# Kernel optimization log

Hardware: AMD Instinct MI355X
Metric: run time of the kernel (lower is better)

## Reference

```python
import jax, jax.numpy as jnp
import numpy as np
from jax import lax

K = 13  # sizearea
DN = ('NCHW', 'OIHW', 'NCHW')


def conv(x, W, b):
    y = lax.conv_general_dilated(x, W, (1, 1), 'SAME', dimension_numbers=DN)
    return y + b[None, :, None, None]


def setup_inputs() -> dict:
    key = jax.random.key(0)
    ks = jax.random.split(key, 4)
    x = jax.random.normal(ks[0], (8, 1, 256, 256), dtype=jnp.float32)
    W1 = jax.random.normal(ks[1], (64, 1, 3, 3), dtype=jnp.float32) * 0.1
    b1 = jnp.zeros((64,), dtype=jnp.float32)
    W2 = jax.random.normal(ks[2], (64, 64, 3, 3), dtype=jnp.float32) * 0.05
    b2 = jnp.zeros((64,), dtype=jnp.float32)
    W3 = jax.random.normal(ks[3], (K * K, 64, 3, 3), dtype=jnp.float32) * 0.05
    b3 = jnp.zeros((K * K,), dtype=jnp.float32)
    return {'x': x, 'W1': W1, 'b1': b1, 'W2': W2, 'b2': b2, 'W3': W3, 'b3': b3}


def reference(x, W1, b1, W2, b2, W3, b3):
    # weight-predicting CNN (sar_data=False -> x used directly)
    h = jax.nn.relu(conv(x, W1, b1))
    h = jax.nn.relu(conv(h, W2, b2))
    w = conv(h, W3, b3)                       # (B, K*K, H, W)

    B, C, H, Wd = x.shape                     # C == 1
    # w.permute(0,2,3,1).view(B,1,H,W,K,K)
    wr = jnp.transpose(w, (0, 2, 3, 1)).reshape(B, 1, H, Wd, K, K)

    Ho, Wo = H - K + 1, Wd - K + 1            # unfold with stride 1, no pad
    pr, pc = (H - Ho) // 2, (Wd - Wo) // 2    # center-crop of weight maps
    wc = wr[:, :, pr:H - pr, pc:Wd - pc]      # (B,1,Ho,Wo,K,K)

    # patches[b,0,i,j,u,v] = x[b,0,i+u,j+v]  (C=1, so channel-major flatten is just (kh,kw))
    patches = lax.conv_general_dilated_patches(
        x, (K, K), (1, 1), 'VALID', dimension_numbers=DN)   # (B, K*K, Ho, Wo)
    patches = patches.reshape(B, 1, K, K, Ho, Wo).transpose(0, 1, 4, 5, 2, 3)

    # per-pixel weighted sum over the KxK window
    y = jnp.einsum('bchwuv,bchwuv->bchw', patches, wc)       # (B,1,Ho,Wo)
    return y
```

## Files before the change

### kernel.cpp

```cpp
#include <hip/hip_runtime.h>

#define HW 256
#define BATCH 8
#define C 64
#define HO 244
#define NPAD 192
#define KTOT 576

typedef __bf16 bf16x8 __attribute__((ext_vector_type(8)));
typedef float f32x16 __attribute__((ext_vector_type(16)));
typedef float f32x2 __attribute__((ext_vector_type(2)));
typedef unsigned short us8 __attribute__((ext_vector_type(8)));

__device__ inline unsigned short fbf(float f) {
    return __builtin_bit_cast(unsigned short, (__bf16)f);
}

__device__ inline float bf2f(unsigned short s) {
    union { unsigned int u; float f; } c;
    c.u = ((unsigned int)s) << 16;
    return c.f;
}

__global__ __launch_bounds__(256) void repack_w_kernel(
    const float* __restrict__ W2, const float* __restrict__ W3,
    unsigned short* __restrict__ B2g, unsigned short* __restrict__ B3g)
{
    int idx = blockIdx.x * 256 + threadIdx.x;
    if (idx < 36 * 2 * C * 8) {
        int e = idx & 7;
        int r = idx >> 3;
        int n = r & 63;
        int s = r >> 6;
        int khalf = s & 1;
        int kstep = s >> 1;
        int chunk = kstep >> 2, ks = kstep & 3;
        int ci = ks * 16 + khalf * 8 + e;
        B2g[idx] = fbf(W2[((size_t)n * C + ci) * 9 + chunk]);
    } else {
        int j = idx - 36 * 2 * C * 8;
        if (j >= 36 * 2 * NPAD * 8) return;
        int e = j & 7;
        int r = j >> 3;
        int n = r % NPAD;
        int s = r / NPAD;
        int khalf = s & 1;
        int kstep = s >> 1;
        int chunk = kstep >> 2, ks = kstep & 3;
        int ci = ks * 16 + khalf * 8 + e;
        float v = (n < 169) ? W3[((size_t)n * C + ci) * 9 + chunk] : 0.f;
        B3g[j] = fbf(v);
    }
}

__global__ __launch_bounds__(256, 3) void conv2_fused_kernel(
    const float* __restrict__ x, const float* __restrict__ W1,
    const float* __restrict__ b1, const unsigned short* __restrict__ W2r,
    const float* __restrict__ b2, unsigned short* __restrict__ h2)
{
    __shared__ unsigned short Ash[396 * 66];
    __shared__ unsigned short Xsh[8 * 68];

    const int t = threadIdx.x;
    const int lane = t & 63;
    const int wave = t >> 6;
    const int b  = blockIdx.z;
    const int h0 = blockIdx.y * 4;
    const int w0 = blockIdx.x * 64;

    const int col   = lane & 31;
    const int khalf = lane >> 5;
    const int mrow_base = wave * 64;

    const float* __restrict__ xplane = x + ((size_t)b << 16);
#pragma unroll
    for (int it = 0; it < 3; ++it) {
        int li = it * 256 + t;
        if (li < 8 * 68) {
            int rr = li / 68, cc = li - rr * 68;
            int hh = h0 - 2 + rr, ww = w0 - 2 + cc;
            bool ok = (hh >= 0) && (hh < HW) && (ww >= 0) && (ww < HW);
            Xsh[li] = ok ? fbf(xplane[hh * HW + ww]) : (unsigned short)0;
        }
    }

    const int g4 = t & 15;
    f32x2 w01[9], w23[9];
    f32x2 bia01, bia23;
    bia01[0] = b1[g4 * 4 + 0]; bia01[1] = b1[g4 * 4 + 1];
    bia23[0] = b1[g4 * 4 + 2]; bia23[1] = b1[g4 * 4 + 3];
#pragma unroll
    for (int q = 0; q < 9; ++q) {
        w01[q][0] = W1[(g4 * 4 + 0) * 9 + q];
        w01[q][1] = W1[(g4 * 4 + 1) * 9 + q];
        w23[q][0] = W1[(g4 * 4 + 2) * 9 + q];
        w23[q][1] = W1[(g4 * 4 + 3) * 9 + q];
    }

    __syncthreads();

    for (int it = 0; it < 25; ++it) {
        int li = it * 256 + t;
        if (li < 6336) {
            int p = li >> 4;
            int pr = p / 66, pc = p - pr * 66;
            int hh = h0 - 1 + pr, ww = w0 - 1 + pc;
            unsigned short ov[4];
            if (hh >= 0 && hh < HW && ww >= 0 && ww < HW) {
                const unsigned short* xb = Xsh + pr * 68 + pc;
                f32x2 a01 = bia01, a23 = bia23;
#pragma unroll
                for (int i = 0; i < 3; ++i)
#pragma unroll
                    for (int j = 0; j < 3; ++j) {
                        float xv = bf2f(xb[i * 68 + j]);
                        f32x2 xv2; xv2[0] = xv; xv2[1] = xv;
                        a01 += xv2 * w01[i * 3 + j];
                        a23 += xv2 * w23[i * 3 + j];
                    }
                ov[0] = fbf(fmaxf(a01[0], 0.f));
                ov[1] = fbf(fmaxf(a01[1], 0.f));
                ov[2] = fbf(fmaxf(a23[0], 0.f));
                ov[3] = fbf(fmaxf(a23[1], 0.f));
            } else {
#pragma unroll
                for (int u = 0; u < 4; ++u) ov[u] = 0;
            }
            *(uint2*)(Ash + p * 66 + g4 * 4) = *(uint2*)ov;
        }
    }

    const unsigned short* bbase = W2r + ((size_t)khalf * C + col) * 8;
    us8 bcur0 = *(const us8*)(bbase);
    us8 bcur1 = *(const us8*)(bbase + 32 * 8);
    us8 bnx0  = *(const us8*)(bbase + (size_t)(2 * C * 8));
    us8 bnx1  = *(const us8*)(bbase + (size_t)(2 * C * 8) + 32 * 8);

    f32x16 acc[2][2];
#pragma unroll
    for (int ai = 0; ai < 2; ++ai)
#pragma unroll
        for (int nb = 0; nb < 2; ++nb)
#pragma unroll
            for (int r = 0; r < 16; ++r) acc[ai][nb][r] = 0.f;

    __syncthreads();

#pragma unroll
    for (int kstep = 0; kstep < 36; ++kstep) {
        const int chunk = kstep >> 2, ks = kstep & 3;
        const int ii = chunk / 3, jj = chunk - ii * 3;
        const int pixbase = (wave + ii) * 66 + jj;
        us8 bn0, bn1;
        if (kstep + 2 < 36) {
            const unsigned short* bp = bbase + (size_t)(kstep + 2) * (2 * C * 8);
            bn0 = *(const us8*)(bp);
            bn1 = *(const us8*)(bp + 32 * 8);
        }
        const int koff = ks * 16 + khalf * 8;
        bf16x8 a0 = __builtin_bit_cast(bf16x8, *(const us8*)(Ash + (pixbase + col) * 66 + koff));
        bf16x8 a1 = __builtin_bit_cast(bf16x8, *(const us8*)(Ash + (pixbase + col + 32) * 66 + koff));
        bf16x8 v0 = __builtin_bit_cast(bf16x8, bcur0);
        bf16x8 v1 = __builtin_bit_cast(bf16x8, bcur1);
        acc[0][0] = __builtin_amdgcn_mfma_f32_32x32x16_bf16(a0, v0, acc[0][0], 0, 0, 0);
        acc[0][1] = __builtin_amdgcn_mfma_f32_32x32x16_bf16(a0, v1, acc[0][1], 0, 0, 0);
        acc[1][0] = __builtin_amdgcn_mfma_f32_32x32x16_bf16(a1, v0, acc[1][0], 0, 0, 0);
        acc[1][1] = __builtin_amdgcn_mfma_f32_32x32x16_bf16(a1, v1, acc[1][1], 0, 0, 0);
        bcur0 = bnx0; bcur1 = bnx1;
        bnx0 = bn0; bnx1 = bn1;
    }

#pragma unroll
    for (int nb = 0; nb < 2; ++nb) {
        const int n = nb * 32 + col;
        const float bias = b2[n];
#pragma unroll
        for (int ai = 0; ai < 2; ++ai) {
#pragma unroll
            for (int r = 0; r < 16; ++r) {
                int m = mrow_base + ai * 32 + (r & 3) + ((r >> 2) << 3) + (khalf << 2);
                int h = h0 + (m >> 6), w = w0 + (m & 63);
                float val = fmaxf(acc[ai][nb][r] + bias, 0.f);
                h2[(((size_t)b * HW + h) * HW + w) * C + n] = fbf(val);
            }
        }
    }
}

__global__ __launch_bounds__(512, 3) void conv3_mfma_kernel(
    const float* __restrict__ x, const unsigned short* __restrict__ h2,
    const unsigned short* __restrict__ Bg, const float* __restrict__ b3,
    float* __restrict__ y)
{
    __shared__ unsigned short Ash[396 * 72];
    __shared__ float Xsh[16 * 77];
    __shared__ float red[8][64];

    const int t = threadIdx.x;
    const int lane = t & 63;
    const int wave = t >> 6;
    const int b   = blockIdx.z;
    const int ho0 = blockIdx.y * 4;
    const int wo0 = blockIdx.x * 64;

    const int col   = lane & 31;
    const int khalf = lane >> 5;
    const int rsel      = wave >> 1;
    const int mrow_base = rsel * 64;
    const int nbase     = (wave & 1) * 96;

    f32x16 acc[2][3];
#pragma unroll
    for (int mi = 0; mi < 2; ++mi)
#pragma unroll
        for (int ni = 0; ni < 3; ++ni)
#pragma unroll
            for (int r = 0; r < 16; ++r) acc[mi][ni][r] = 0.f;

#pragma unroll
    for (int it = 0; it < 7; ++it) {
        int li = it * 512 + t;
        if (li < 396 * 8) {
            int p = li >> 3, g = li & 7;
            int row = p / 66, cl = p - row * 66;
            int ww = wo0 + 5 + cl; ww = ww < 255 ? ww : 255;
            size_t src = (((size_t)b * HW + (ho0 + 5 + row)) * HW + ww) * C + g * 8;
            *(uint4*)(Ash + p * 72 + g * 8) = *(const uint4*)(h2 + src);
        }
    }
    {
        const float* __restrict__ xplane = x + ((size_t)b << 16);
#pragma unroll
        for (int it = 0; it < 3; ++it) {
            int li = it * 512 + t;
            if (li < 16 * 76) {
                int rr = li / 76, cc = li - rr * 76;
                int ww = wo0 + cc; ww = ww < 255 ? ww : 255;
                Xsh[rr * 77 + cc] = xplane[(ho0 + rr) * HW + ww];
            }
        }
    }

    const unsigned short* bbase = Bg + ((size_t)khalf * NPAD + nbase + col) * 8;
    us8 bcur0 = *(const us8*)(bbase);
    us8 bcur1 = *(const us8*)(bbase + 32 * 8);
    us8 bcur2 = *(const us8*)(bbase + 64 * 8);
    us8 bnx0  = *(const us8*)(bbase + (size_t)(2 * NPAD * 8));
    us8 bnx1  = *(const us8*)(bbase + (size_t)(2 * NPAD * 8) + 32 * 8);
    us8 bnx2  = *(const us8*)(bbase + (size_t)(2 * NPAD * 8) + 64 * 8);

    __syncthreads();

#pragma unroll
    for (int kstep = 0; kstep < 36; ++kstep) {
        const int chunk = kstep >> 2, ks = kstep & 3;
        const int ii = chunk / 3, jj = chunk - ii * 3;
        const int pixbase = (rsel + ii) * 66 + jj;
        us8 bn0, bn1, bn2;
        if (kstep + 2 < 36) {
            const unsigned short* bp = bbase + (size_t)(kstep + 2) * (2 * NPAD * 8);
            bn0 = *(const us8*)(bp);
            bn1 = *(const us8*)(bp + 32 * 8);
            bn2 = *(const us8*)(bp + 64 * 8);
        }
        const int koff = ks * 16 + khalf * 8;
        bf16x8 a0 = __builtin_bit_cast(bf16x8, *(const us8*)(Ash + (pixbase + col) * 72 + koff));
        bf16x8 a1 = __builtin_bit_cast(bf16x8, *(const us8*)(Ash + (pixbase + col + 32) * 72 + koff));
        bf16x8 v0 = __builtin_bit_cast(bf16x8, bcur0);
        bf16x8 v1 = __builtin_bit_cast(bf16x8, bcur1);
        bf16x8 v2 = __builtin_bit_cast(bf16x8, bcur2);
        acc[0][0] = __builtin_amdgcn_mfma_f32_32x32x16_bf16(a0, v0, acc[0][0], 0, 0, 0);
        acc[0][1] = __builtin_amdgcn_mfma_f32_32x32x16_bf16(a0, v1, acc[0][1], 0, 0, 0);
        acc[0][2] = __builtin_amdgcn_mfma_f32_32x32x16_bf16(a0, v2, acc[0][2], 0, 0, 0);
        acc[1][0] = __builtin_amdgcn_mfma_f32_32x32x16_bf16(a1, v0, acc[1][0], 0, 0, 0);
        acc[1][1] = __builtin_amdgcn_mfma_f32_32x32x16_bf16(a1, v1, acc[1][1], 0, 0, 0);
        acc[1][2] = __builtin_amdgcn_mfma_f32_32x32x16_bf16(a1, v2, acc[1][2], 0, 0, 0);
        bcur0 = bnx0; bcur1 = bnx1; bcur2 = bnx2;
        bnx0 = bn0; bnx1 = bn1; bnx2 = bn2;
    }

    int   qv[3], uo[3], vo[3];
    float b3v[3];
#pragma unroll
    for (int ni = 0; ni < 3; ++ni) {
        int q = nbase + ni * 32 + col;
        qv[ni] = q;
        int u = q / 13;
        uo[ni] = u;
        vo[ni] = q - u * 13;
        b3v[ni] = (q < 169) ? b3[q] : 0.f;
    }

    float partial[2][16];
#pragma unroll
    for (int mi = 0; mi < 2; ++mi)
#pragma unroll
        for (int r = 0; r < 16; ++r) {
            int mrow = mi * 32 + (r & 3) + ((r >> 2) << 3) + (khalf << 2);
            bool wok = (wo0 + mrow) < HO;
            float p = 0.f;
#pragma unroll
            for (int ni = 0; ni < 3; ++ni) {
                if (qv[ni] < 169 && wok) {
                    float s = acc[mi][ni][r] + b3v[ni];
                    p += s * Xsh[(rsel + uo[ni]) * 77 + mrow + vo[ni]];
                }
            }
            partial[mi][r] = p;
        }

#pragma unroll
    for (int mi = 0; mi < 2; ++mi)
#pragma unroll
        for (int r = 0; r < 16; ++r) {
            float p = partial[mi][r];
#pragma unroll
            for (int d = 1; d < 32; d <<= 1) p += __shfl_xor(p, d, 64);
            partial[mi][r] = p;
        }

    if (col == 0) {
#pragma unroll
        for (int mi = 0; mi < 2; ++mi)
#pragma unroll
            for (int r = 0; r < 16; ++r) {
                int mrow = mi * 32 + (r & 3) + ((r >> 2) << 3) + (khalf << 2);
                red[wave][mrow] = partial[mi][r];
            }
    }
    __syncthreads();

    if (t < 256) {
        int row_sel = t >> 6, m = t & 63;
        float val = red[row_sel * 2][m] + red[row_sel * 2 + 1][m];
        int wo = wo0 + m, ho = ho0 + row_sel;
        if (wo < HO)
            y[((size_t)b * HO + ho) * HO + wo] = val;
    }
}

extern "C" void kernel_launch(void* const* d_in, const int* in_sizes, int n_in,
                              void* d_out, int out_size, void* d_ws, size_t ws_size,
                              hipStream_t stream) {
    const float* x  = (const float*)d_in[0];
    const float* W1 = (const float*)d_in[1];
    const float* b1 = (const float*)d_in[2];
    const float* W2 = (const float*)d_in[3];
    const float* b2 = (const float*)d_in[4];
    const float* W3 = (const float*)d_in[5];
    const float* b3 = (const float*)d_in[6];
    float* out = (float*)d_out;

    unsigned short* h2  = (unsigned short*)d_ws;
    unsigned short* W2r = h2 + (size_t)BATCH * HW * HW * C;
    unsigned short* W3r = W2r + (size_t)36 * 2 * C * 8;

    repack_w_kernel<<<576, 256, 0, stream>>>(W2, W3, W2r, W3r);
    conv2_fused_kernel<<<dim3(4, 64, 8), 256, 0, stream>>>(x, W1, b1, W2r, b2, h2);
    conv3_mfma_kernel<<<dim3(4, 61, 8), 512, 0, stream>>>(x, h2, W3r, b3, out);
}
```

Before: 240.3 us.

## Stage conv3 weight slices through double-buffered LDS and raise MFMA priority

In the conv3 kernel, each wave no longer loads its own copy of the weight (B) fragments from global memory. Six waves now cooperatively copy each k-step's weight slice into a double-buffered shared-memory array, which also replaces the separate reduction scratch. The intent is to cut redundant global and L2 traffic, since four waves previously fetched the same B data. The cost is a __syncthreads on every one of the 36 k-steps plus extra LDS reads. s_setprio is also wrapped around the MFMA groups in both conv2 and conv3.

```diff
diff --git a/kernel.cpp b/kernel.cpp
--- a/kernel.cpp
+++ b/kernel.cpp
@@ -162,10 +162,12 @@
         bf16x8 a1 = __builtin_bit_cast(bf16x8, *(const us8*)(Ash + (pixbase + col + 32) * 66 + koff));
         bf16x8 v0 = __builtin_bit_cast(bf16x8, bcur0);
         bf16x8 v1 = __builtin_bit_cast(bf16x8, bcur1);
+        __builtin_amdgcn_s_setprio(1);
         acc[0][0] = __builtin_amdgcn_mfma_f32_32x32x16_bf16(a0, v0, acc[0][0], 0, 0, 0);
         acc[0][1] = __builtin_amdgcn_mfma_f32_32x32x16_bf16(a0, v1, acc[0][1], 0, 0, 0);
         acc[1][0] = __builtin_amdgcn_mfma_f32_32x32x16_bf16(a1, v0, acc[1][0], 0, 0, 0);
         acc[1][1] = __builtin_amdgcn_mfma_f32_32x32x16_bf16(a1, v1, acc[1][1], 0, 0, 0);
+        __builtin_amdgcn_s_setprio(0);
         bcur0 = bnx0; bcur1 = bnx1;
         bnx0 = bn0; bnx1 = bn1;
     }
@@ -194,7 +196,8 @@
 {
     __shared__ unsigned short Ash[396 * 72];
     __shared__ float Xsh[16 * 77];
-    __shared__ float red[8][64];
+    __shared__ unsigned short Bsh[2 * 3072];
+    float (*red)[64] = (float (*)[64])Bsh;
 
     const int t = threadIdx.x;
     const int lane = t & 63;
@@ -206,7 +209,6 @@
     const int col   = lane & 31;
     const int khalf = lane >> 5;
     const int rsel      = wave >> 1;
-    const int mrow_base = rsel * 64;
     const int nbase     = (wave & 1) * 96;
 
     f32x16 acc[2][3];
@@ -241,42 +243,50 @@
         }
     }
 
-    const unsigned short* bbase = Bg + ((size_t)khalf * NPAD + nbase + col) * 8;
-    us8 bcur0 = *(const us8*)(bbase);
-    us8 bcur1 = *(const us8*)(bbase + 32 * 8);
-    us8 bcur2 = *(const us8*)(bbase + 64 * 8);
-    us8 bnx0  = *(const us8*)(bbase + (size_t)(2 * NPAD * 8));
-    us8 bnx1  = *(const us8*)(bbase + (size_t)(2 * NPAD * 8) + 32 * 8);
-    us8 bnx2  = *(const us8*)(bbase + (size_t)(2 * NPAD * 8) + 64 * 8);
+    const unsigned short* bgs = Bg + wave * 512 + lane * 8;
+    unsigned short*       bls = Bsh + wave * 512 + lane * 8;
+    us8 btmp;
+    if (wave < 6) {
+        us8 t0 = *(const us8*)(bgs);
+        *(us8*)(bls) = t0;
+        btmp = *(const us8*)(bgs + 3072);
+    }
 
     __syncthreads();
 
 #pragma unroll
     for (int kstep = 0; kstep < 36; ++kstep) {
-        const int chunk = kstep >> 2, ks = kstep & 3;
-        const int ii = chunk / 3, jj = chunk - ii * 3;
+        if (wave < 6) {
+            if (kstep + 1 < 36)
+                *(us8*)(bls + ((kstep + 1) & 1) * 3072) = btmp;
+            if (kstep + 2 < 36)
+                btmp = *(const us8*)(bgs + (size_t)(kstep + 2) * 3072);
+        }
+
+        const int chnk = kstep >> 2, ks = kstep & 3;
+        const int ii = chnk / 3, jj = chnk - ii * 3;
         const int pixbase = (rsel + ii) * 66 + jj;
-        us8 bn0, bn1, bn2;
-        if (kstep + 2 < 36) {
-            const unsigned short* bp = bbase + (size_t)(kstep + 2) * (2 * NPAD * 8);
-            bn0 = *(const us8*)(bp);
-            bn1 = *(const us8*)(bp + 32 * 8);
-            bn2 = *(const us8*)(bp + 64 * 8);
-        }
         const int koff = ks * 16 + khalf * 8;
+
+        const unsigned short* bb =
+            Bsh + (kstep & 1) * 3072 + ((khalf * NPAD + nbase + col) * 8);
+
         bf16x8 a0 = __builtin_bit_cast(bf16x8, *(const us8*)(Ash + (pixbase + col) * 72 + koff));
         bf16x8 a1 = __builtin_bit_cast(bf16x8, *(const us8*)(Ash + (pixbase + col + 32) * 72 + koff));
-        bf16x8 v0 = __builtin_bit_cast(bf16x8, bcur0);
-        bf16x8 v1 = __builtin_bit_cast(bf16x8, bcur1);
-        bf16x8 v2 = __builtin_bit_cast(bf16x8, bcur2);
+        bf16x8 v0 = __builtin_bit_cast(bf16x8, *(const us8*)(bb));
+        bf16x8 v1 = __builtin_bit_cast(bf16x8, *(const us8*)(bb + 32 * 8));
+        bf16x8 v2 = __builtin_bit_cast(bf16x8, *(const us8*)(bb + 64 * 8));
+
+        __builtin_amdgcn_s_setprio(1);
         acc[0][0] = __builtin_amdgcn_mfma_f32_32x32x16_bf16(a0, v0, acc[0][0], 0, 0, 0);
         acc[0][1] = __builtin_amdgcn_mfma_f32_32x32x16_bf16(a0, v1, acc[0][1], 0, 0, 0);
         acc[0][2] = __builtin_amdgcn_mfma_f32_32x32x16_bf16(a0, v2, acc[0][2], 0, 0, 0);
         acc[1][0] = __builtin_amdgcn_mfma_f32_32x32x16_bf16(a1, v0, acc[1][0], 0, 0, 0);
         acc[1][1] = __builtin_amdgcn_mfma_f32_32x32x16_bf16(a1, v1, acc[1][1], 0, 0, 0);
         acc[1][2] = __builtin_amdgcn_mfma_f32_32x32x16_bf16(a1, v2, acc[1][2], 0, 0, 0);
-        bcur0 = bnx0; bcur1 = bnx1; bcur2 = bnx2;
-        bnx0 = bn0; bnx1 = bn1; bnx2 = bn2;
+        __builtin_amdgcn_s_setprio(0);
+
+        __syncthreads();
     }
 
     int   qv[3], uo[3], vo[3];
```

New measurement: 291.3 us. 1.21x slower.
